# Optimization experiments

Measured on AMD Instinct MI355X. Metric: run time of the kernel, lower is better.

The kernel has to match this reference:

```python
import jax, jax.numpy as jnp
import numpy as np

B, C, N, M = 8, 128, 2048, 512

def setup_inputs() -> dict:
    key = jax.random.key(0)
    k1, k2, k3, k4 = jax.random.split(key, 4)
    scale = 1.0 / np.sqrt(C)
    x = jax.random.normal(k1, (B, C, N), dtype=jnp.float32)
    # conv1d with kernel size 1 and no bias == channel-mixing matmul, weight [C_out, C_in]
    Wq = jax.random.normal(k2, (C, C), dtype=jnp.float32) * scale
    Wk = jax.random.normal(k3, (C, C), dtype=jnp.float32) * scale
    Wv = jax.random.normal(k4, (C, C), dtype=jnp.float32) * scale
    return {"x": x, "Wq": Wq, "Wk": Wk, "Wv": Wv, "npts_ds": M}

def reference(x, Wq, Wk, Wv, npts_ds):
    # q,k,v: [B,C,N] via 1x1 conv == einsum over input channels
    q = jnp.einsum('oc,bcn->bon', Wq, x)
    k = jnp.einsum('oc,bcn->bon', Wk, x)
    v = jnp.einsum('oc,bcn->bon', Wv, x)
    # energy: [B,N,N] = q^T k (contract channel dim)
    energy = jnp.einsum('bcn,bcm->bnm', q, k)
    scale_factor = jnp.sqrt(jnp.asarray(q.shape[-2], dtype=energy.dtype))  # sqrt(C)
    attention = jax.nn.softmax(energy / scale_factor, axis=-1)  # [B,N,N]
    selection = jnp.sum(attention, axis=-2)  # [B,N] column sums
    _, idx = jax.lax.top_k(selection, npts_ds)  # [B,M]
    # gather selected attention rows: [B,M,N]
    scores = jnp.take_along_axis(attention, idx[:, :, None], axis=1)
    # weighted sum of values: [B,M,C]
    out = jnp.einsum('bmn,bcn->bcm', scores, v)  # [B,C,M]
    return out
```

## Files before the change

kernel.cpp:

```cpp
#include <hip/hip_runtime.h>
#include <math.h>

namespace {
constexpr int B = 8, C = 128, N = 2048, M = 512;
constexpr int NSPLIT = 8;
constexpr int MBLK = 16;
constexpr float INV_SQRT_C = 0.08838834764831845f;
}

typedef __attribute__((ext_vector_type(8))) short short8;
typedef __attribute__((ext_vector_type(16))) float f32x16;
typedef unsigned short ushort_t;
typedef unsigned int u32;

__device__ inline ushort_t f2bf(float f) {
  union { float f; u32 u; } a; a.f = f;
  u32 r = a.u + 0x7fffu + ((a.u >> 16) & 1u);
  return (ushort_t)(r >> 16);
}
__device__ inline float bf2f(ushort_t h) {
  union { u32 u; float f; } a; a.u = ((u32)h) << 16; return a.f;
}

__global__ __launch_bounds__(256) void qkv_kernel(
    const float* __restrict__ x, const float* __restrict__ Wq,
    const float* __restrict__ Wk, const float* __restrict__ Wv,
    ushort_t* __restrict__ split, ushort_t* __restrict__ vbf) {
  const size_t TERM = (size_t)B * N * C;
  int kc = blockIdx.x;
  int o0 = kc * 8;
  int n = blockIdx.y * 256 + threadIdx.x;
  int b = blockIdx.z;
  const float* xb = x + (size_t)b * C * N + n;
  float aq[8] = {}, ak[8] = {}, av[8] = {};
  #pragma unroll 4
  for (int c = 0; c < C; ++c) {
    float xv = xb[(size_t)c * N];
    #pragma unroll
    for (int j = 0; j < 8; ++j) {
      aq[j] = fmaf(Wq[(o0 + j) * C + c], xv, aq[j]);
      ak[j] = fmaf(Wk[(o0 + j) * C + c], xv, ak[j]);
      av[j] = fmaf(Wv[(o0 + j) * C + c], xv, av[j]);
    }
  }
  #pragma unroll
  for (int j = 0; j < 8; ++j)
    vbf[((size_t)b * C + o0 + j) * N + n] = f2bf(av[j]);
  size_t rowoff = ((size_t)b * 16 + kc) * (size_t)N * 8 + (size_t)n * 8;
  #pragma unroll
  for (int tt = 0; tt < 3; ++tt) {
    short8 qv, kv;
    #pragma unroll
    for (int j = 0; j < 8; ++j) {
      ushort_t h = f2bf(aq[j]); qv[j] = (short)h; aq[j] -= bf2f(h);
      h = f2bf(ak[j]);          kv[j] = (short)h; ak[j] -= bf2f(h);
    }
    *(short8*)&split[tt * TERM + rowoff]       = qv;
    *(short8*)&split[(3 + tt) * TERM + rowoff] = kv;
  }
}

__global__ __launch_bounds__(256) void energy_kernel(
    const ushort_t* __restrict__ split,
    float* __restrict__ Ae, float* __restrict__ rowpart) {
  __shared__ float red[128][64];
  __shared__ float red2[128][2];
  const size_t TERM = (size_t)B * N * C;
  const size_t ROW8 = (size_t)N * 8;
  int t = threadIdx.x;
  int lane = t & 63, w = t >> 6;
  int wn = w & 1, wm = w >> 1;
  int lin = blockIdx.y * 16 + blockIdx.x;
  int st = lin >> 4, wi = lin & 15;
  int mb = (st & 3) * 4 + (wi & 3);
  int nb = (st >> 2) * 4 + (wi >> 2);
  int m0 = mb * 128, n0 = nb * 128, b = blockIdx.z;
  int lr = lane & 31, lq = lane >> 5;
  size_t kbase = ((size_t)b * 16 + lq) * ROW8;
  const ushort_t* Abase = split + kbase + (size_t)(n0 + wn * 64 + lr) * 8;
  const ushort_t* Bbase = split + 3 * TERM + kbase + (size_t)(m0 + wm * 64 + lr) * 8;
  f32x16 acc[2][2] = {};
  #pragma unroll
  for (int s = 0; s < 8; ++s) {
    size_t so = (size_t)s * 2 * ROW8;
    short8 aT[3][2], bT[3][2];
    #pragma unroll
    for (int tt = 0; tt < 3; ++tt)
      #pragma unroll
      for (int i = 0; i < 2; ++i) {
        aT[tt][i] = *(const short8*)(Abase + tt * TERM + so + i * 256);
        bT[tt][i] = *(const short8*)(Bbase + tt * TERM + so + i * 256);
      }
    #pragma unroll
    for (int mt = 0; mt < 2; ++mt)
      #pragma unroll
      for (int nt = 0; nt < 2; ++nt) {
        acc[mt][nt] = __builtin_amdgcn_mfma_f32_32x32x16_bf16(aT[0][mt], bT[0][nt], acc[mt][nt], 0, 0, 0);
        acc[mt][nt] = __builtin_amdgcn_mfma_f32_32x32x16_bf16(aT[1][mt], bT[0][nt], acc[mt][nt], 0, 0, 0);
        acc[mt][nt] = __builtin_amdgcn_mfma_f32_32x32x16_bf16(aT[0][mt], bT[1][nt], acc[mt][nt], 0, 0, 0);
        acc[mt][nt] = __builtin_amdgcn_mfma_f32_32x32x16_bf16(aT[2][mt], bT[0][nt], acc[mt][nt], 0, 0, 0);
        acc[mt][nt] = __builtin_amdgcn_mfma_f32_32x32x16_bf16(aT[1][mt], bT[1][nt], acc[mt][nt], 0, 0, 0);
        acc[mt][nt] = __builtin_amdgcn_mfma_f32_32x32x16_bf16(aT[0][mt], bT[2][nt], acc[mt][nt], 0, 0, 0);
      }
  }
  int lc = lr;
  #pragma unroll
  for (int mt = 0; mt < 2; ++mt) {
    #pragma unroll
    for (int reg = 0; reg < 16; ++reg) {
      int row = (reg & 3) + 8 * (reg >> 2) + 4 * lq;
      int rloc = wn * 64 + mt * 32 + row;
      float e0 = expf(acc[mt][0][reg] * INV_SQRT_C);
      float e1 = expf(acc[mt][1][reg] * INV_SQRT_C);
      float* pA = Ae + ((size_t)b * N + n0 + rloc) * N + m0 + wm * 64 + lc;
      pA[0] = e0; pA[32] = e1;
      red[rloc][wm * 32 + lc] = e0 + e1;
    }
  }
  __syncthreads();
  {
    int row = t >> 1, h = t & 1;
    float ssum = 0.f;
    #pragma unroll
    for (int j0 = 0; j0 < 32; ++j0) {
      int j = (j0 + (t & 31)) & 31;
      ssum += red[row][h * 32 + j];
    }
    red2[row][h] = ssum;
  }
  __syncthreads();
  if (t < 128)
    rowpart[(size_t)mb * (B * N) + b * N + n0 + t] = red2[t][0] + red2[t][1];
}

__global__ __launch_bounds__(256) void colsum_kernel(
    const float* __restrict__ Ae, const float* __restrict__ rowpart,
    float* __restrict__ selpart) {
  __shared__ float sinv[256];
  int t = threadIdx.x;
  int m = blockIdx.x * 256 + t;
  int nch = blockIdx.y, b = blockIdx.z;
  int n0 = nch * (N / 8);
  {
    int n = n0 + t;
    float s = 0.f;
    #pragma unroll
    for (int sl = 0; sl < MBLK; ++sl)
      s += rowpart[(size_t)sl * (B * N) + b * N + n];
    sinv[t] = 1.0f / s;
  }
  __syncthreads();
  const float* Ab = Ae + (size_t)b * N * N;
  float acc = 0.f;
  #pragma unroll 8
  for (int n = n0; n < n0 + N / 8; ++n)
    acc = fmaf(Ab[(size_t)n * N + m], sinv[n - n0], acc);
  selpart[(size_t)nch * (B * N) + b * N + m] = acc;
}

__global__ __launch_bounds__(256) void topk_kernel(
    const float* __restrict__ selpart, int* __restrict__ idx) {
  __shared__ float s[N];
  __shared__ int rsum[64][4];
  int b = blockIdx.y;
  int t = threadIdx.x;
  for (int i = t; i < N; i += 256) {
    float v_ = 0.f;
    #pragma unroll
    for (int nch = 0; nch < 8; ++nch)
      v_ += selpart[(size_t)nch * (B * N) + b * N + i];
    s[i] = v_;
  }
  __syncthreads();
  int i = blockIdx.x * 64 + (t & 63);
  int jc = t >> 6;
  float val = s[i];
  int r = 0;
  for (int j = jc * 512; j < jc * 512 + 512; ++j) {
    float sj = s[j];
    r += (sj > val || (sj == val && j < i)) ? 1 : 0;
  }
  rsum[t & 63][jc] = r;
  __syncthreads();
  if (t < 64) {
    int rank = rsum[t][0] + rsum[t][1] + rsum[t][2] + rsum[t][3];
    if (rank < M) idx[b * M + rank] = blockIdx.x * 64 + t;
  }
}

__global__ __launch_bounds__(256) void out_kernel(
    const float* __restrict__ Ae, const float* __restrict__ rowpart,
    const ushort_t* __restrict__ vbf, const int* __restrict__ idx,
    float* __restrict__ part) {
  __shared__ ushort_t sc[64][72];
  __shared__ ushort_t vt[128][72];
  __shared__ int ridx[64];
  __shared__ float rinv[64];
  int t = threadIdx.x;
  int m0 = blockIdx.x * 64;
  int ns = blockIdx.y;
  int b = blockIdx.z;
  if (t < 64) {
    int r = idx[b * M + m0 + t];
    ridx[t] = r;
    float s = 0.f;
    #pragma unroll
    for (int sl = 0; sl < MBLK; ++sl)
      s += rowpart[(size_t)sl * (B * N) + b * N + r];
    rinv[t] = 1.0f / s;
  }
  __syncthreads();
  int lane = t & 63, w = t >> 6;
  int wc = w & 1, wm = w >> 1;
  int lr = lane & 31, lq = lane >> 5;
  f32x16 acc[2] = {};
  int nbeg = ns * (N / NSPLIT);
  for (int kb = 0; kb < N / NSPLIT; kb += 64) {
    __syncthreads();
    #pragma unroll
    for (int it = 0; it < 16; ++it) {
      int ii = it * 256 + t;
      int r = ii >> 6, cn = ii & 63;
      float sv = Ae[((size_t)b * N + ridx[r]) * N + nbeg + kb + cn] * rinv[r];
      sc[r][cn] = f2bf(sv);
    }
    #pragma unroll
    for (int it = 0; it < 4; ++it) {
      int u = it * 256 + t;
      int r = u >> 3, seg = u & 7;
      *(short8*)&vt[r][seg * 8] =
          *(const short8*)&vbf[((size_t)b * C + r) * N + nbeg + kb + seg * 8];
    }
    __syncthreads();
    #pragma unroll
    for (int ks = 0; ks < 4; ++ks) {
      short8 bf_ = *(const short8*)&sc[wm * 32 + lr][ks * 16 + lq * 8];
      #pragma unroll
      for (int ct = 0; ct < 2; ++ct) {
        short8 af = *(const short8*)&vt[wc * 64 + ct * 32 + lr][ks * 16 + lq * 8];
        acc[ct] = __builtin_amdgcn_mfma_f32_32x32x16_bf16(af, bf_, acc[ct], 0, 0, 0);
      }
    }
  }
  float* pb = part + ((size_t)ns * B + b) * C * M;
  #pragma unroll
  for (int ct = 0; ct < 2; ++ct) {
    #pragma unroll
    for (int reg = 0; reg < 16; ++reg) {
      int crow = wc * 64 + ct * 32 + (reg & 3) + 8 * (reg >> 2) + 4 * lq;
      pb[(size_t)crow * M + m0 + wm * 32 + lr] = acc[ct][reg];
    }
  }
}

__global__ __launch_bounds__(256) void reduce_kernel(
    const float* __restrict__ part, float* __restrict__ out) {
  int i = (blockIdx.x * 256 + threadIdx.x) * 4;
  float4 a = make_float4(0.f, 0.f, 0.f, 0.f);
  #pragma unroll
  for (int ns = 0; ns < NSPLIT; ++ns) {
    float4 p = *(const float4*)&part[(size_t)ns * (B * C * M) + i];
    a.x += p.x; a.y += p.y; a.z += p.z; a.w += p.w;
  }
  *(float4*)&out[i] = a;
}

extern "C" void kernel_launch(void* const* d_in, const int* in_sizes, int n_in,
                              void* d_out, int out_size, void* d_ws, size_t ws_size,
                              hipStream_t stream) {
  const float* x  = (const float*)d_in[0];
  const float* Wq = (const float*)d_in[1];
  const float* Wk = (const float*)d_in[2];
  const float* Wv = (const float*)d_in[3];
  float* out = (float*)d_out;

  const size_t TSZ = (size_t)B * N * C;
  ushort_t* split = (ushort_t*)d_ws;
  ushort_t* vbf   = split + 6 * TSZ;
  float* Ae       = (float*)(vbf + TSZ);
  float* rowpart  = Ae + (size_t)B * N * N;
  float* selpart  = rowpart + (size_t)MBLK * B * N;
  int*   idx      = (int*)(selpart + (size_t)8 * B * N);
  float* part     = (float*)split;

  qkv_kernel<<<dim3(16, N / 256, B), 256, 0, stream>>>(x, Wq, Wk, Wv, split, vbf);
  energy_kernel<<<dim3(N / 128, N / 128, B), 256, 0, stream>>>(split, Ae, rowpart);
  colsum_kernel<<<dim3(N / 256, 8, B), 256, 0, stream>>>(Ae, rowpart, selpart);
  topk_kernel<<<dim3(N / 64, B), 256, 0, stream>>>(selpart, idx);
  out_kernel<<<dim3(M / 64, NSPLIT, B), 256, 0, stream>>>(Ae, rowpart, vbf, idx, part);
  reduce_kernel<<<dim3(B * C * M / 1024), 256, 0, stream>>>(part, out);
}
```

Measured before the change: 236.3 us.

## Fuse colsum, topk, output GEMM and reduce into one cooperative kernel

Merges the four tail kernels into a single cooperative kernel of 512 blocks. Grid-wide syncs replace the kernel boundaries between stages, and the stages share LDS through a union. The aim is to remove launch overhead and inter-kernel gaps. In exchange it adds grid.sync costs and requires all 512 blocks to be co-resident. It also leaves blocks idle during the topk stage, where only 256 are used.

```diff
diff --git a/kernel.cpp b/kernel.cpp
--- a/kernel.cpp
+++ b/kernel.cpp
@@ -1,5 +1,8 @@
 #include <hip/hip_runtime.h>
+#include <hip/hip_cooperative_groups.h>
 #include <math.h>
+
+namespace cg = cooperative_groups;
 
 namespace {
 constexpr int B = 8, C = 128, N = 2048, M = 512;
@@ -133,136 +136,140 @@
     rowpart[(size_t)mb * (B * N) + b * N + n0 + t] = red2[t][0] + red2[t][1];
 }
 
-__global__ __launch_bounds__(256) void colsum_kernel(
+__global__ __launch_bounds__(256) void tail_kernel(
     const float* __restrict__ Ae, const float* __restrict__ rowpart,
-    float* __restrict__ selpart) {
-  __shared__ float sinv[256];
+    const ushort_t* __restrict__ vbf,
+    float* __restrict__ selpart, int* __restrict__ idx,
+    float* __restrict__ part, float* __restrict__ out) {
+  __shared__ union {
+    struct { float sinv[256]; } cs;
+    struct { float s[N]; int rsum[64][4]; } tk;
+    struct { ushort_t sc[64][72]; ushort_t vt[128][72];
+             int ridx[64]; float rinv[64]; } ot;
+  } sh;
+  cg::grid_group grid = cg::this_grid();
+  int blk = blockIdx.x;
   int t = threadIdx.x;
-  int m = blockIdx.x * 256 + t;
-  int nch = blockIdx.y, b = blockIdx.z;
-  int n0 = nch * (N / 8);
+
   {
-    int n = n0 + t;
-    float s = 0.f;
-    #pragma unroll
-    for (int sl = 0; sl < MBLK; ++sl)
-      s += rowpart[(size_t)sl * (B * N) + b * N + n];
-    sinv[t] = 1.0f / s;
-  }
-  __syncthreads();
-  const float* Ab = Ae + (size_t)b * N * N;
-  float acc = 0.f;
-  #pragma unroll 8
-  for (int n = n0; n < n0 + N / 8; ++n)
-    acc = fmaf(Ab[(size_t)n * N + m], sinv[n - n0], acc);
-  selpart[(size_t)nch * (B * N) + b * N + m] = acc;
-}
-
-__global__ __launch_bounds__(256) void topk_kernel(
-    const float* __restrict__ selpart, int* __restrict__ idx) {
-  __shared__ float s[N];
-  __shared__ int rsum[64][4];
-  int b = blockIdx.y;
-  int t = threadIdx.x;
-  for (int i = t; i < N; i += 256) {
-    float v_ = 0.f;
-    #pragma unroll
-    for (int nch = 0; nch < 8; ++nch)
-      v_ += selpart[(size_t)nch * (B * N) + b * N + i];
-    s[i] = v_;
-  }
-  __syncthreads();
-  int i = blockIdx.x * 64 + (t & 63);
-  int jc = t >> 6;
-  float val = s[i];
-  int r = 0;
-  for (int j = jc * 512; j < jc * 512 + 512; ++j) {
-    float sj = s[j];
-    r += (sj > val || (sj == val && j < i)) ? 1 : 0;
-  }
-  rsum[t & 63][jc] = r;
-  __syncthreads();
-  if (t < 64) {
-    int rank = rsum[t][0] + rsum[t][1] + rsum[t][2] + rsum[t][3];
-    if (rank < M) idx[b * M + rank] = blockIdx.x * 64 + t;
-  }
-}
-
-__global__ __launch_bounds__(256) void out_kernel(
-    const float* __restrict__ Ae, const float* __restrict__ rowpart,
-    const ushort_t* __restrict__ vbf, const int* __restrict__ idx,
-    float* __restrict__ part) {
-  __shared__ ushort_t sc[64][72];
-  __shared__ ushort_t vt[128][72];
-  __shared__ int ridx[64];
-  __shared__ float rinv[64];
-  int t = threadIdx.x;
-  int m0 = blockIdx.x * 64;
-  int ns = blockIdx.y;
-  int b = blockIdx.z;
-  if (t < 64) {
-    int r = idx[b * M + m0 + t];
-    ridx[t] = r;
-    float s = 0.f;
-    #pragma unroll
-    for (int sl = 0; sl < MBLK; ++sl)
-      s += rowpart[(size_t)sl * (B * N) + b * N + r];
-    rinv[t] = 1.0f / s;
-  }
-  __syncthreads();
-  int lane = t & 63, w = t >> 6;
-  int wc = w & 1, wm = w >> 1;
-  int lr = lane & 31, lq = lane >> 5;
-  f32x16 acc[2] = {};
-  int nbeg = ns * (N / NSPLIT);
-  for (int kb = 0; kb < N / NSPLIT; kb += 64) {
+    int bx = blk & 7, nch = (blk >> 3) & 7, b = blk >> 6;
+    int m = bx * 256 + t;
+    int n0 = nch * (N / 8);
+    {
+      int n = n0 + t;
+      float s = 0.f;
+      #pragma unroll
+      for (int sl = 0; sl < MBLK; ++sl)
+        s += rowpart[(size_t)sl * (B * N) + b * N + n];
+      sh.cs.sinv[t] = 1.0f / s;
+    }
     __syncthreads();
-    #pragma unroll
-    for (int it = 0; it < 16; ++it) {
-      int ii = it * 256 + t;
-      int r = ii >> 6, cn = ii & 63;
-      float sv = Ae[((size_t)b * N + ridx[r]) * N + nbeg + kb + cn] * rinv[r];
-      sc[r][cn] = f2bf(sv);
-    }
-    #pragma unroll
-    for (int it = 0; it < 4; ++it) {
-      int u = it * 256 + t;
-      int r = u >> 3, seg = u & 7;
-      *(short8*)&vt[r][seg * 8] =
-          *(const short8*)&vbf[((size_t)b * C + r) * N + nbeg + kb + seg * 8];
+    const float* Ab = Ae + (size_t)b * N * N;
+    float acc = 0.f;
+    #pragma unroll 8
+    for (int n = n0; n < n0 + N / 8; ++n)
+      acc = fmaf(Ab[(size_t)n * N + m], sh.cs.sinv[n - n0], acc);
+    selpart[(size_t)nch * (B * N) + b * N + m] = acc;
+  }
+  __threadfence();
+  grid.sync();
+
+  if (blk < 256) {
+    int bx = blk & 31, b = blk >> 5;
+    for (int i = t; i < N; i += 256) {
+      float v_ = 0.f;
+      #pragma unroll
+      for (int nch = 0; nch < 8; ++nch)
+        v_ += selpart[(size_t)nch * (B * N) + b * N + i];
+      sh.tk.s[i] = v_;
     }
     __syncthreads();
-    #pragma unroll
-    for (int ks = 0; ks < 4; ++ks) {
-      short8 bf_ = *(const short8*)&sc[wm * 32 + lr][ks * 16 + lq * 8];
-      #pragma unroll
-      for (int ct = 0; ct < 2; ++ct) {
-        short8 af = *(const short8*)&vt[wc * 64 + ct * 32 + lr][ks * 16 + lq * 8];
-        acc[ct] = __builtin_amdgcn_mfma_f32_32x32x16_bf16(af, bf_, acc[ct], 0, 0, 0);
-      }
-    }
-  }
-  float* pb = part + ((size_t)ns * B + b) * C * M;
-  #pragma unroll
-  for (int ct = 0; ct < 2; ++ct) {
-    #pragma unroll
-    for (int reg = 0; reg < 16; ++reg) {
-      int crow = wc * 64 + ct * 32 + (reg & 3) + 8 * (reg >> 2) + 4 * lq;
-      pb[(size_t)crow * M + m0 + wm * 32 + lr] = acc[ct][reg];
-    }
-  }
-}
-
-__global__ __launch_bounds__(256) void reduce_kernel(
-    const float* __restrict__ part, float* __restrict__ out) {
-  int i = (blockIdx.x * 256 + threadIdx.x) * 4;
-  float4 a = make_float4(0.f, 0.f, 0.f, 0.f);
-  #pragma unroll
-  for (int ns = 0; ns < NSPLIT; ++ns) {
-    float4 p = *(const float4*)&part[(size_t)ns * (B * C * M) + i];
-    a.x += p.x; a.y += p.y; a.z += p.z; a.w += p.w;
-  }
-  *(float4*)&out[i] = a;
+    int i = bx * 64 + (t & 63);
+    int jc = t >> 6;
+    float val = sh.tk.s[i];
+    int r = 0;
+    for (int j = jc * 512; j < jc * 512 + 512; ++j) {
+      float sj = sh.tk.s[j];
+      r += (sj > val || (sj == val && j < i)) ? 1 : 0;
+    }
+    sh.tk.rsum[t & 63][jc] = r;
+    __syncthreads();
+    if (t < 64) {
+      int rank = sh.tk.rsum[t][0] + sh.tk.rsum[t][1] + sh.tk.rsum[t][2] + sh.tk.rsum[t][3];
+      if (rank < M) idx[b * M + rank] = bx * 64 + t;
+    }
+  }
+  __threadfence();
+  grid.sync();
+
+  {
+    int mx = blk & 7, ns = (blk >> 3) & 7, b = blk >> 6;
+    int m0 = mx * 64;
+    if (t < 64) {
+      int r = idx[b * M + m0 + t];
+      sh.ot.ridx[t] = r;
+      float s = 0.f;
+      #pragma unroll
+      for (int sl = 0; sl < MBLK; ++sl)
+        s += rowpart[(size_t)sl * (B * N) + b * N + r];
+      sh.ot.rinv[t] = 1.0f / s;
+    }
+    __syncthreads();
+    int lane = t & 63, w = t >> 6;
+    int wc = w & 1, wm = w >> 1;
+    int lr = lane & 31, lq = lane >> 5;
+    f32x16 acc[2] = {};
+    int nbeg = ns * (N / NSPLIT);
+    for (int kb = 0; kb < N / NSPLIT; kb += 64) {
+      __syncthreads();
+      #pragma unroll
+      for (int it = 0; it < 16; ++it) {
+        int ii = it * 256 + t;
+        int r = ii >> 6, cn = ii & 63;
+        float sv = Ae[((size_t)b * N + sh.ot.ridx[r]) * N + nbeg + kb + cn] * sh.ot.rinv[r];
+        sh.ot.sc[r][cn] = f2bf(sv);
+      }
+      #pragma unroll
+      for (int it = 0; it < 4; ++it) {
+        int u = it * 256 + t;
+        int r = u >> 3, seg = u & 7;
+        *(short8*)&sh.ot.vt[r][seg * 8] =
+            *(const short8*)&vbf[((size_t)b * C + r) * N + nbeg + kb + seg * 8];
+      }
+      __syncthreads();
+      #pragma unroll
+      for (int ks = 0; ks < 4; ++ks) {
+        short8 bf_ = *(const short8*)&sh.ot.sc[wm * 32 + lr][ks * 16 + lq * 8];
+        #pragma unroll
+        for (int ct = 0; ct < 2; ++ct) {
+          short8 af = *(const short8*)&sh.ot.vt[wc * 64 + ct * 32 + lr][ks * 16 + lq * 8];
+          acc[ct] = __builtin_amdgcn_mfma_f32_32x32x16_bf16(af, bf_, acc[ct], 0, 0, 0);
+        }
+      }
+    }
+    float* pb = part + ((size_t)ns * B + b) * C * M;
+    #pragma unroll
+    for (int ct = 0; ct < 2; ++ct) {
+      #pragma unroll
+      for (int reg = 0; reg < 16; ++reg) {
+        int crow = wc * 64 + ct * 32 + (reg & 3) + 8 * (reg >> 2) + 4 * lq;
+        pb[(size_t)crow * M + m0 + wm * 32 + lr] = acc[ct][reg];
+      }
+    }
+  }
+  __threadfence();
+  grid.sync();
+
+  {
+    int i = (blk * 256 + t) * 4;
+    float4 a = make_float4(0.f, 0.f, 0.f, 0.f);
+    #pragma unroll
+    for (int ns = 0; ns < NSPLIT; ++ns) {
+      float4 p = *(const float4*)&part[(size_t)ns * (B * C * M) + i];
+      a.x += p.x; a.y += p.y; a.z += p.z; a.w += p.w;
+    }
+    *(float4*)&out[i] = a;
+  }
 }
 
 extern "C" void kernel_launch(void* const* d_in, const int* in_sizes, int n_in,
@@ -285,8 +292,9 @@
 
   qkv_kernel<<<dim3(16, N / 256, B), 256, 0, stream>>>(x, Wq, Wk, Wv, split, vbf);
   energy_kernel<<<dim3(N / 128, N / 128, B), 256, 0, stream>>>(split, Ae, rowpart);
-  colsum_kernel<<<dim3(N / 256, 8, B), 256, 0, stream>>>(Ae, rowpart, selpart);
-  topk_kernel<<<dim3(N / 64, B), 256, 0, stream>>>(selpart, idx);
-  out_kernel<<<dim3(M / 64, NSPLIT, B), 256, 0, stream>>>(Ae, rowpart, vbf, idx, part);
-  reduce_kernel<<<dim3(B * C * M / 1024), 256, 0, stream>>>(part, out);
-}
+
+  void* args[] = {(void*)&Ae, (void*)&rowpart, (void*)&vbf,
+                  (void*)&selpart, (void*)&idx, (void*)&part, (void*)&out};
+  hipLaunchCooperativeKernel((const void*)tail_kernel, dim3(512), dim3(256),
+                             args, 0, stream);
+}
```

New measurement: 542.6 us. 130% more time.
